# Optimization experiments

Hardware: AMD Instinct MI355X
Metric: run time of the kernel (lower is better)

Reference implementation:

```python
import jax, jax.numpy as jnp
import numpy as np

B, S, H, D = 4, 2048, 16, 64
E = H * D  # embedding_dim = 1024


def setup_inputs() -> dict:
    key = jax.random.key(0)
    ks = jax.random.split(key, 5)
    scale = 1.0 / np.sqrt(E)
    return {
        "x": jax.random.normal(ks[0], (B, S, E), dtype=jnp.float32),
        "wq": jax.random.normal(ks[1], (E, E), dtype=jnp.float32) * scale,
        "wk": jax.random.normal(ks[2], (E, E), dtype=jnp.float32) * scale,
        "wv": jax.random.normal(ks[3], (E, E), dtype=jnp.float32) * scale,
        "wo": jax.random.normal(ks[4], (E, E), dtype=jnp.float32) * scale,
    }


def reference(x, wq, wk, wv, wo):
    b, s, e = x.shape
    # nn.Linear: y = x @ W^T (no bias; use_bias=False)
    q = (x @ wq.T).reshape(b, s, H, D)
    k = (x @ wk.T).reshape(b, s, H, D)
    v = (x @ wv.T).reshape(b, s, H, D)
    # NOTE: original scales by sqrt(embedding_dim), not sqrt(head_dim)
    scores = jnp.einsum("bqhd,bkhd->bhqk", q, k) / jnp.sqrt(jnp.float32(e))
    causal = jnp.tril(jnp.ones((s, s), dtype=bool))  # mask[:s,:s]
    scores = jnp.where(causal, scores, -jnp.inf)
    attn = jax.nn.softmax(scores, axis=-1)
    out = jnp.einsum("bhql,blhd->bqhd", attn, v).reshape(b, s, e)
    return out @ wo.T
```

## Files before the change

### kernel.cpp

```cpp
#include <hip/hip_runtime.h>
#include <hip/hip_bf16.h>

#define E_DIM 1024
#define NHEAD 16
#define HDIM  64
#define BATCH 4
#define SEQ   2048
#define RQKV  (3 * E_DIM)

typedef __attribute__((ext_vector_type(8))) short bf16x8;
typedef __attribute__((ext_vector_type(4))) float f32x4;
typedef __attribute__((ext_vector_type(16))) float f32x16;

#define SCL2 0.04508422f

static __device__ __forceinline__ unsigned short bits_of(__hip_bfloat16 h) {
    return *reinterpret_cast<unsigned short*>(&h);
}

static __device__ __forceinline__ void gload_lds16(const void* g, void* l) {
    __builtin_amdgcn_global_load_lds(
        (__attribute__((address_space(1))) void*)g,
        (__attribute__((address_space(3))) void*)l, 16, 0, 0);
}

static __device__ __forceinline__ unsigned cvt_pk_bf16(float a, float b) {
    unsigned r;
    asm("v_cvt_pk_bf16_f32 %0, %1, %2" : "=v"(r) : "v"(a), "v"(b));
    return r;
}

static __device__ __forceinline__ float exp2_raw(float x) {
    float r;
    asm("v_exp_f32 %0, %1" : "=v"(r) : "v"(x));
    return r;
}

__global__ void cast_all_kernel(
    const float* __restrict__ x,  const float* __restrict__ wq,
    const float* __restrict__ wk, const float* __restrict__ wv,
    const float* __restrict__ wo,
    __hip_bfloat16* __restrict__ xb, __hip_bfloat16* __restrict__ wqkvb,
    __hip_bfloat16* __restrict__ wob) {
    const int NX4 = (BATCH * SEQ * E_DIM) / 4;
    const int NW4 = (E_DIM * E_DIM) / 4;
    int id = blockIdx.x * 256 + threadIdx.x;

    const float* in;
    __hip_bfloat16* out;
    float scl = 1.0f;
    if (id < NX4) {
        in = x; out = xb;
    } else {
        const int r = id - NX4;
        const int wsel = r >> 18;
        id = r & (NW4 - 1);
        switch (wsel) {
            case 0: in = wq; out = wqkvb;            scl = SCL2; break;
            case 1: in = wk; out = wqkvb + NW4 * 4;  break;
            case 2: in = wv; out = wqkvb + NW4 * 8;  break;
            default: in = wo; out = wob;             break;
        }
    }
    float4 v = reinterpret_cast<const float4*>(in)[id];
    ushort4 u;
    u.x = bits_of(__float2bfloat16(v.x * scl));
    u.y = bits_of(__float2bfloat16(v.y * scl));
    u.z = bits_of(__float2bfloat16(v.z * scl));
    u.w = bits_of(__float2bfloat16(v.w * scl));
    reinterpret_cast<ushort4*>(out)[id] = u;
}

template<int FN, int OUT_F32>
__global__ __launch_bounds__(512) void gemm_ph(
    const __hip_bfloat16* __restrict__ A,
    const __hip_bfloat16* __restrict__ Bw,
    void* __restrict__ Cv,
    int M, int N, int K) {
    constexpr int BN = FN * 64;
    __shared__ __align__(16) __hip_bfloat16 As[2][128 * 64];
    __shared__ __align__(16) __hip_bfloat16 Bs[2][BN * 64];

    const int nbx = gridDim.x;
    const int lin = blockIdx.y * nbx + blockIdx.x;
    const int cpx = (nbx * gridDim.y) >> 3;
    const int swz = (lin & 7) * cpx + (lin >> 3);
    const int mBase = (swz / nbx) * 128, nBase = (swz % nbx) * BN;

    const int t = threadIdx.x, lane = t & 63, w = t >> 6;
    const int wr = w >> 2, wc = w & 3;
    const int lr = lane & 15;
    const int lkb = (lane >> 4) * 16;

    f32x4 acc[4][FN];
#pragma unroll
    for (int i = 0; i < 4; ++i)
#pragma unroll
        for (int j = 0; j < FN; ++j) acc[i][j] = (f32x4){0.f, 0.f, 0.f, 0.f};

    const int NKT = K >> 6;

    auto STAGE = [&](int kt, int b) {
#pragma unroll
        for (int i = 0; i < 2; ++i) {
            const int q = i * 512 + t;
            const int r = q >> 3, cb = (q & 7) * 16;
            const char* src = (const char*)A +
                ((size_t)(mBase + r) * K + kt * 64) * 2 + (cb ^ ((r & 7) << 4));
            gload_lds16(src, (char*)&As[b][0] + q * 16);
        }
#pragma unroll
        for (int i = 0; i < FN; ++i) {
            const int q = i * 512 + t;
            const int r = q >> 3, cb = (q & 7) * 16;
            const char* src = (const char*)Bw +
                ((size_t)(nBase + r) * K + kt * 64) * 2 + (cb ^ ((r & 7) << 4));
            gload_lds16(src, (char*)&Bs[b][0] + q * 16);
        }
    };

    STAGE(0, 0);
    for (int kt = 0; kt < NKT; ++kt) {
        const int buf = kt & 1;
        asm volatile("s_waitcnt vmcnt(0)" ::: "memory");
        __builtin_amdgcn_s_barrier();
        __builtin_amdgcn_sched_barrier(0);

        bf16x8 bfr[FN][2];
#pragma unroll
        for (int fn = 0; fn < FN; ++fn)
#pragma unroll
            for (int ks = 0; ks < 2; ++ks) {
                const int R = wc * (FN * 16) + fn * 16 + lr;
                const int addr = R * 128 + ((ks * 64 + lkb) ^ ((R & 7) << 4));
                bfr[fn][ks] = *reinterpret_cast<const bf16x8*>(
                    (const char*)&Bs[buf][0] + addr);
            }
        {
            bf16x8 af[2][2];
#pragma unroll
            for (int f = 0; f < 2; ++f)
#pragma unroll
                for (int ks = 0; ks < 2; ++ks) {
                    const int R = wr * 64 + f * 16 + lr;
                    const int addr = R * 128 + ((ks * 64 + lkb) ^ ((R & 7) << 4));
                    af[f][ks] = *reinterpret_cast<const bf16x8*>(
                        (const char*)&As[buf][0] + addr);
                }
            if (kt + 1 < NKT) STAGE(kt + 1, buf ^ 1);
            __builtin_amdgcn_s_setprio(1);
#pragma unroll
            for (int f = 0; f < 2; ++f)
#pragma unroll
                for (int fn = 0; fn < FN; ++fn)
#pragma unroll
                    for (int ks = 0; ks < 2; ++ks)
                        acc[f][fn] = __builtin_amdgcn_mfma_f32_16x16x32_bf16(
                            af[f][ks], bfr[fn][ks], acc[f][fn], 0, 0, 0);
            __builtin_amdgcn_s_setprio(0);
        }
        {
            bf16x8 af[2][2];
#pragma unroll
            for (int f = 0; f < 2; ++f)
#pragma unroll
                for (int ks = 0; ks < 2; ++ks) {
                    const int R = wr * 64 + (f + 2) * 16 + lr;
                    const int addr = R * 128 + ((ks * 64 + lkb) ^ ((R & 7) << 4));
                    af[f][ks] = *reinterpret_cast<const bf16x8*>(
                        (const char*)&As[buf][0] + addr);
                }
            __builtin_amdgcn_s_setprio(1);
#pragma unroll
            for (int f = 0; f < 2; ++f)
#pragma unroll
                for (int fn = 0; fn < FN; ++fn)
#pragma unroll
                    for (int ks = 0; ks < 2; ++ks)
                        acc[f + 2][fn] = __builtin_amdgcn_mfma_f32_16x16x32_bf16(
                            af[f][ks], bfr[fn][ks], acc[f + 2][fn], 0, 0, 0);
            __builtin_amdgcn_s_setprio(0);
        }
    }

#pragma unroll
    for (int fm = 0; fm < 4; ++fm)
#pragma unroll
        for (int fn = 0; fn < FN; ++fn)
#pragma unroll
            for (int v = 0; v < 4; ++v) {
                const int row = mBase + wr * 64 + fm * 16 + (lane >> 4) * 4 + v;
                const int col = nBase + wc * (FN * 16) + fn * 16 + lr;
                if (OUT_F32)
                    ((float*)Cv)[(size_t)row * N + col] = acc[fm][fn][v];
                else
                    ((__hip_bfloat16*)Cv)[(size_t)row * N + col] =
                        __float2bfloat16(acc[fm][fn][v]);
            }
}

__global__ __launch_bounds__(256) void attn_kernel(
    const __hip_bfloat16* __restrict__ QKV,
    __hip_bfloat16* __restrict__ O) {
    __shared__ __align__(16) __hip_bfloat16 Kl[2][64][64];
    __shared__ __align__(16) __hip_bfloat16 Vt[2][64][64];

    const int t = threadIdx.x, w = t >> 6, lane = t & 63;
    const int lq = lane & 31, hi = lane >> 5;

    const int id = blockIdx.x;
    const int c = id & 7, k = id >> 3;
    const int bh = (k & 7) * 8 + c;
    const int qq = k >> 3;
    const int qb = (qq & 4) ? (qq < 8 ? qq + 4 : qq - 12) : 15 - qq;
    const int b = bh >> 4, h = bh & 15;

    const size_t rb = (size_t)b * SEQ;
    const __hip_bfloat16* Qg = QKV + rb * RQKV + h * HDIM;
    const __hip_bfloat16* Kg = QKV + rb * RQKV + E_DIM + h * HDIM;
    const __hip_bfloat16* Vg = QKV + rb * RQKV + 2 * E_DIM + h * HDIM;

    const int kst_row  = w * 16 + (lane >> 3);
    const int kst_slot = lane & 7;
    const int vkp = t & 31, vd0 = (t >> 5) * 8;

    const int qw0 = qb * 128 + w * 32;
    const int qg  = qw0 + lq;

    bf16x8 aq[4];
#pragma unroll
    for (int d0 = 0; d0 < 4; ++d0)
        aq[d0] = *reinterpret_cast<const bf16x8*>(
            Qg + (size_t)qg * RQKV + d0 * 16 + hi * 8);

    f32x16 oa[2];
#pragma unroll
    for (int m = 0; m < 2; ++m)
#pragma unroll
        for (int r = 0; r < 16; ++r) oa[m][r] = 0.f;
    float l_run = 0.f;

    const int NP = qb + 1;
    for (int pr = 0; pr < NP; ++pr) {
        const int k0a = pr * 128;
        __syncthreads();

#pragma unroll
        for (int half = 0; half < 2; ++half)
#pragma unroll
            for (int i = 0; i < 2; ++i) {
                const int r = kst_row + i * 8;
                const char* src =
                    (const char*)(Kg + (size_t)(k0a + half * 64 + r) * RQKV) +
                    ((kst_slot * 16) ^ ((r & 7) << 4));
                gload_lds16(src, &Kl[half][w * 16 + i * 8][0]);
            }
        {
            const __hip_bfloat16* vp0 =
                Vg + (size_t)(k0a + 2 * vkp) * RQKV + vd0;
            const __hip_bfloat16* vp1 = vp0 + (size_t)64 * RQKV;
            union { bf16x8 v; unsigned u[4]; } A0, B0, A1, B1;
            A0.v = *reinterpret_cast<const bf16x8*>(vp0);
            B0.v = *reinterpret_cast<const bf16x8*>(vp0 + RQKV);
            A1.v = *reinterpret_cast<const bf16x8*>(vp1);
            B1.v = *reinterpret_cast<const bf16x8*>(vp1 + RQKV);
            char* vt0 = reinterpret_cast<char*>(&Vt[0][0][0]);
            char* vt1 = reinterpret_cast<char*>(&Vt[1][0][0]);
#pragma unroll
            for (int jw = 0; jw < 4; ++jw) {
                const int da = vd0 + 2 * jw, db = da + 1;
                const int offa = da * 128 + ((vkp * 4) ^ ((da & 7) << 4));
                const int offb = db * 128 + ((vkp * 4) ^ ((db & 7) << 4));
                *reinterpret_cast<unsigned*>(vt0 + offa) =
                    __builtin_amdgcn_perm(B0.u[jw], A0.u[jw], 0x05040100u);
                *reinterpret_cast<unsigned*>(vt0 + offb) =
                    __builtin_amdgcn_perm(B0.u[jw], A0.u[jw], 0x07060302u);
                *reinterpret_cast<unsigned*>(vt1 + offa) =
                    __builtin_amdgcn_perm(B1.u[jw], A1.u[jw], 0x05040100u);
                *reinterpret_cast<unsigned*>(vt1 + offb) =
                    __builtin_amdgcn_perm(B1.u[jw], A1.u[jw], 0x07060302u);
            }
        }
        __syncthreads();

#pragma unroll
        for (int half = 0; half < 2; ++half) {
            const int k0 = k0a + half * 64;
            if (k0 > qw0 + 31) continue;

            f32x16 sc2[2];
            const char* klbase = (const char*)&Kl[half][0][0];
#pragma unroll
            for (int tt = 0; tt < 2; ++tt) {
#pragma unroll
                for (int r = 0; r < 16; ++r) sc2[tt][r] = 0.f;
                const int kr = tt * 32 + lq;
                const char* kbase = klbase + kr * 128;
                const int swz = (kr & 7) << 4;
#pragma unroll
                for (int d0 = 0; d0 < 4; ++d0) {
                    bf16x8 ak = *reinterpret_cast<const bf16x8*>(
                        kbase + ((d0 * 32 + hi * 16) ^ swz));
                    sc2[tt] = __builtin_amdgcn_mfma_f32_32x32x16_bf16(
                        ak, aq[d0], sc2[tt], 0, 0, 0);
                }
            }
            if (k0 + 63 > qw0) {
#pragma unroll
                for (int tt = 0; tt < 2; ++tt)
#pragma unroll
                    for (int r = 0; r < 16; ++r) {
                        const int kgl = k0 + tt * 32 +
                                        (r & 3) + 8 * (r >> 2) + 4 * hi;
                        if (kgl > qg) sc2[tt][r] = -1e30f;
                    }
            }
            float rsum = 0.f;
#pragma unroll
            for (int tt = 0; tt < 2; ++tt) {
                float s0 = 0.f, s1 = 0.f, s2 = 0.f, s3 = 0.f;
#pragma unroll
                for (int r = 0; r < 16; r += 4) {
                    float p0 = exp2_raw(sc2[tt][r]);
                    float p1 = exp2_raw(sc2[tt][r + 1]);
                    float p2 = exp2_raw(sc2[tt][r + 2]);
                    float p3 = exp2_raw(sc2[tt][r + 3]);
                    sc2[tt][r] = p0; sc2[tt][r + 1] = p1;
                    sc2[tt][r + 2] = p2; sc2[tt][r + 3] = p3;
                    s0 += p0; s1 += p1; s2 += p2; s3 += p3;
                }
                rsum += (s0 + s1) + (s2 + s3);
            }
            l_run += rsum;

            const char* vtbase = (const char*)&Vt[half][0][0];
#pragma unroll
            for (int tt = 0; tt < 2; ++tt)
#pragma unroll
                for (int sl = 0; sl < 2; ++sl) {
                    const int rbs = sl * 8;
                    const unsigned wA = cvt_pk_bf16(sc2[tt][rbs + 0], sc2[tt][rbs + 1]);
                    const unsigned wB = cvt_pk_bf16(sc2[tt][rbs + 2], sc2[tt][rbs + 3]);
                    const unsigned wC = cvt_pk_bf16(sc2[tt][rbs + 4], sc2[tt][rbs + 5]);
                    const unsigned wD = cvt_pk_bf16(sc2[tt][rbs + 6], sc2[tt][rbs + 7]);
                    const auto pA = __builtin_amdgcn_permlane32_swap(wA, wC, false, false);
                    const auto pB = __builtin_amdgcn_permlane32_swap(wB, wD, false, false);
                    union { unsigned u[4]; bf16x8 v; } pf;
                    pf.u[0] = pA[0]; pf.u[1] = pB[0];
                    pf.u[2] = pA[1]; pf.u[3] = pB[1];
                    const int ks = tt * 2 + sl;
#pragma unroll
                    for (int m = 0; m < 2; ++m) {
                        const int dr = m * 32 + lq;
                        bf16x8 av = *reinterpret_cast<const bf16x8*>(
                            vtbase + dr * 128 +
                            ((ks * 32 + hi * 16) ^ ((dr & 7) << 4)));
                        oa[m] = __builtin_amdgcn_mfma_f32_32x32x16_bf16(
                            av, pf.v, oa[m], 0, 0, 0);
                    }
                }
        }
    }

    l_run += __shfl_xor(l_run, 32);
    const float inv = 1.f / l_run;
    __hip_bfloat16* Orow = O + (rb + qg) * E_DIM + h * HDIM;
#pragma unroll
    for (int m = 0; m < 2; ++m)
#pragma unroll
        for (int q4 = 0; q4 < 4; ++q4) {
            ushort4 pk;
            pk.x = bits_of(__float2bfloat16(oa[m][q4 * 4 + 0] * inv));
            pk.y = bits_of(__float2bfloat16(oa[m][q4 * 4 + 1] * inv));
            pk.z = bits_of(__float2bfloat16(oa[m][q4 * 4 + 2] * inv));
            pk.w = bits_of(__float2bfloat16(oa[m][q4 * 4 + 3] * inv));
            *reinterpret_cast<ushort4*>(Orow + m * 32 + q4 * 8 + 4 * hi) = pk;
        }
}

extern "C" void kernel_launch(void* const* d_in, const int* in_sizes, int n_in,
                              void* d_out, int out_size, void* d_ws, size_t ws_size,
                              hipStream_t stream) {
    const float* x  = (const float*)d_in[0];
    const float* wq = (const float*)d_in[1];
    const float* wk = (const float*)d_in[2];
    const float* wv = (const float*)d_in[3];
    const float* wo = (const float*)d_in[4];

    const size_t SZ_X = (size_t)BATCH * SEQ * E_DIM;
    const size_t SZ_W = (size_t)E_DIM * E_DIM;

    char* p = (char*)d_ws;
    __hip_bfloat16* xb    = (__hip_bfloat16*)p; p += SZ_X * 2;
    __hip_bfloat16* wqkvb = (__hip_bfloat16*)p; p += 3 * SZ_W * 2;
    __hip_bfloat16* wob   = (__hip_bfloat16*)p; p += SZ_W * 2;
    __hip_bfloat16* QKVb  = (__hip_bfloat16*)p; p += SZ_X * 3 * 2;
    __hip_bfloat16* attb  = (__hip_bfloat16*)p; p += SZ_X * 2;

    cast_all_kernel<<<dim3(12288), 256, 0, stream>>>(
        x, wq, wk, wv, wo, xb, wqkvb, wob);

    const int M = BATCH * SEQ;
    gemm_ph<3, 0><<<dim3(RQKV / 192, M / 128), 512, 0, stream>>>(
        xb, wqkvb, QKVb, M, RQKV, E_DIM);

    attn_kernel<<<dim3(1024), 256, 0, stream>>>(QKVb, attb);

    gemm_ph<2, 1><<<dim3(E_DIM / 128, M / 128), 512, 0, stream>>>(
        attb, wob, d_out, M, E_DIM, E_DIM);
}
```

Before: 149.2 us.

## Shrink attention blocks to 64 queries with 2 waves and single K/V tile

Result: slower. 168.7 us (+13.1%).

```diff
diff --git a/kernel.cpp b/kernel.cpp
--- a/kernel.cpp
+++ b/kernel.cpp
@@ -199,20 +199,19 @@
             }
 }
 
-__global__ __launch_bounds__(256) void attn_kernel(
+__global__ __launch_bounds__(128) void attn_kernel(
     const __hip_bfloat16* __restrict__ QKV,
     __hip_bfloat16* __restrict__ O) {
-    __shared__ __align__(16) __hip_bfloat16 Kl[2][64][64];
-    __shared__ __align__(16) __hip_bfloat16 Vt[2][64][64];
+    __shared__ __align__(16) __hip_bfloat16 Kl[64][64];
+    __shared__ __align__(16) __hip_bfloat16 Vt[64][64];
 
     const int t = threadIdx.x, w = t >> 6, lane = t & 63;
     const int lq = lane & 31, hi = lane >> 5;
 
     const int id = blockIdx.x;
-    const int c = id & 7, k = id >> 3;
-    const int bh = (k & 7) * 8 + c;
-    const int qq = k >> 3;
-    const int qb = (qq & 4) ? (qq < 8 ? qq + 4 : qq - 12) : 15 - qq;
+    const int c = id & 7, j = id >> 3;
+    const int bh = (j & 7) * 8 + c;
+    const int qtile = j >> 3;
     const int b = bh >> 4, h = bh & 15;
 
     const size_t rb = (size_t)b * SEQ;
@@ -220,11 +219,10 @@
     const __hip_bfloat16* Kg = QKV + rb * RQKV + E_DIM + h * HDIM;
     const __hip_bfloat16* Vg = QKV + rb * RQKV + 2 * E_DIM + h * HDIM;
 
-    const int kst_row  = w * 16 + (lane >> 3);
-    const int kst_slot = lane & 7;
-    const int vkp = t & 31, vd0 = (t >> 5) * 8;
-
-    const int qw0 = qb * 128 + w * 32;
+    const int vkp = t & 31;
+    const int vdg = (t >> 5) * 16;
+
+    const int qw0 = qtile * 64 + w * 32;
     const int qg  = qw0 + lq;
 
     bf16x8 aq[4];
@@ -240,126 +238,110 @@
         for (int r = 0; r < 16; ++r) oa[m][r] = 0.f;
     float l_run = 0.f;
 
-    const int NP = qb + 1;
-    for (int pr = 0; pr < NP; ++pr) {
-        const int k0a = pr * 128;
+    const int NT = qtile + 1;
+    for (int kt = 0; kt < NT; ++kt) {
+        const int k0 = kt * 64;
         __syncthreads();
 
 #pragma unroll
-        for (int half = 0; half < 2; ++half)
-#pragma unroll
-            for (int i = 0; i < 2; ++i) {
-                const int r = kst_row + i * 8;
-                const char* src =
-                    (const char*)(Kg + (size_t)(k0a + half * 64 + r) * RQKV) +
-                    ((kst_slot * 16) ^ ((r & 7) << 4));
-                gload_lds16(src, &Kl[half][w * 16 + i * 8][0]);
-            }
+        for (int i = 0; i < 4; ++i) {
+            const int r = w * 32 + i * 8 + (lane >> 3);
+            const char* src = (const char*)(Kg + (size_t)(k0 + r) * RQKV) +
+                              (((lane & 7) * 16) ^ ((r & 7) << 4));
+            gload_lds16(src, &Kl[w * 32 + i * 8][0]);
+        }
         {
-            const __hip_bfloat16* vp0 =
-                Vg + (size_t)(k0a + 2 * vkp) * RQKV + vd0;
-            const __hip_bfloat16* vp1 = vp0 + (size_t)64 * RQKV;
-            union { bf16x8 v; unsigned u[4]; } A0, B0, A1, B1;
-            A0.v = *reinterpret_cast<const bf16x8*>(vp0);
-            B0.v = *reinterpret_cast<const bf16x8*>(vp0 + RQKV);
-            A1.v = *reinterpret_cast<const bf16x8*>(vp1);
-            B1.v = *reinterpret_cast<const bf16x8*>(vp1 + RQKV);
-            char* vt0 = reinterpret_cast<char*>(&Vt[0][0][0]);
-            char* vt1 = reinterpret_cast<char*>(&Vt[1][0][0]);
-#pragma unroll
-            for (int jw = 0; jw < 4; ++jw) {
-                const int da = vd0 + 2 * jw, db = da + 1;
-                const int offa = da * 128 + ((vkp * 4) ^ ((da & 7) << 4));
-                const int offb = db * 128 + ((vkp * 4) ^ ((db & 7) << 4));
-                *reinterpret_cast<unsigned*>(vt0 + offa) =
-                    __builtin_amdgcn_perm(B0.u[jw], A0.u[jw], 0x05040100u);
-                *reinterpret_cast<unsigned*>(vt0 + offb) =
-                    __builtin_amdgcn_perm(B0.u[jw], A0.u[jw], 0x07060302u);
-                *reinterpret_cast<unsigned*>(vt1 + offa) =
-                    __builtin_amdgcn_perm(B1.u[jw], A1.u[jw], 0x05040100u);
-                *reinterpret_cast<unsigned*>(vt1 + offb) =
-                    __builtin_amdgcn_perm(B1.u[jw], A1.u[jw], 0x07060302u);
+            const __hip_bfloat16* vp = Vg + (size_t)(k0 + 2 * vkp) * RQKV + vdg;
+            char* vt = reinterpret_cast<char*>(&Vt[0][0]);
+#pragma unroll
+            for (int o = 0; o < 2; ++o) {
+                union { bf16x8 v; unsigned u[4]; } Aa, Bb;
+                Aa.v = *reinterpret_cast<const bf16x8*>(vp + o * 8);
+                Bb.v = *reinterpret_cast<const bf16x8*>(vp + RQKV + o * 8);
+#pragma unroll
+                for (int jw = 0; jw < 4; ++jw) {
+                    const int da = vdg + o * 8 + 2 * jw, db = da + 1;
+                    *reinterpret_cast<unsigned*>(
+                        vt + da * 128 + ((vkp * 4) ^ ((da & 7) << 4))) =
+                        __builtin_amdgcn_perm(Bb.u[jw], Aa.u[jw], 0x05040100u);
+                    *reinterpret_cast<unsigned*>(
+                        vt + db * 128 + ((vkp * 4) ^ ((db & 7) << 4))) =
+                        __builtin_amdgcn_perm(Bb.u[jw], Aa.u[jw], 0x07060302u);
+                }
             }
         }
         __syncthreads();
 
-#pragma unroll
-        for (int half = 0; half < 2; ++half) {
-            const int k0 = k0a + half * 64;
-            if (k0 > qw0 + 31) continue;
-
-            f32x16 sc2[2];
-            const char* klbase = (const char*)&Kl[half][0][0];
-#pragma unroll
-            for (int tt = 0; tt < 2; ++tt) {
-#pragma unroll
-                for (int r = 0; r < 16; ++r) sc2[tt][r] = 0.f;
-                const int kr = tt * 32 + lq;
-                const char* kbase = klbase + kr * 128;
-                const int swz = (kr & 7) << 4;
-#pragma unroll
-                for (int d0 = 0; d0 < 4; ++d0) {
-                    bf16x8 ak = *reinterpret_cast<const bf16x8*>(
-                        kbase + ((d0 * 32 + hi * 16) ^ swz));
-                    sc2[tt] = __builtin_amdgcn_mfma_f32_32x32x16_bf16(
-                        ak, aq[d0], sc2[tt], 0, 0, 0);
-                }
-            }
-            if (k0 + 63 > qw0) {
-#pragma unroll
-                for (int tt = 0; tt < 2; ++tt)
-#pragma unroll
-                    for (int r = 0; r < 16; ++r) {
-                        const int kgl = k0 + tt * 32 +
-                                        (r & 3) + 8 * (r >> 2) + 4 * hi;
-                        if (kgl > qg) sc2[tt][r] = -1e30f;
-                    }
-            }
-            float rsum = 0.f;
-#pragma unroll
-            for (int tt = 0; tt < 2; ++tt) {
-                float s0 = 0.f, s1 = 0.f, s2 = 0.f, s3 = 0.f;
-#pragma unroll
-                for (int r = 0; r < 16; r += 4) {
-                    float p0 = exp2_raw(sc2[tt][r]);
-                    float p1 = exp2_raw(sc2[tt][r + 1]);
-                    float p2 = exp2_raw(sc2[tt][r + 2]);
-                    float p3 = exp2_raw(sc2[tt][r + 3]);
-                    sc2[tt][r] = p0; sc2[tt][r + 1] = p1;
-                    sc2[tt][r + 2] = p2; sc2[tt][r + 3] = p3;
-                    s0 += p0; s1 += p1; s2 += p2; s3 += p3;
-                }
-                rsum += (s0 + s1) + (s2 + s3);
-            }
-            l_run += rsum;
-
-            const char* vtbase = (const char*)&Vt[half][0][0];
+        f32x16 sc2[2];
+#pragma unroll
+        for (int tt = 0; tt < 2; ++tt) {
+#pragma unroll
+            for (int r = 0; r < 16; ++r) sc2[tt][r] = 0.f;
+            const int kr = tt * 32 + lq;
+            const char* kbase =
+                reinterpret_cast<const char*>(&Kl[0][0]) + kr * 128;
+            const int swz = (kr & 7) << 4;
+#pragma unroll
+            for (int d0 = 0; d0 < 4; ++d0) {
+                bf16x8 ak = *reinterpret_cast<const bf16x8*>(
+                    kbase + ((d0 * 32 + hi * 16) ^ swz));
+                sc2[tt] = __builtin_amdgcn_mfma_f32_32x32x16_bf16(
+                    ak, aq[d0], sc2[tt], 0, 0, 0);
+            }
+        }
+        if (k0 + 63 > qw0) {
 #pragma unroll
             for (int tt = 0; tt < 2; ++tt)
 #pragma unroll
-                for (int sl = 0; sl < 2; ++sl) {
-                    const int rbs = sl * 8;
-                    const unsigned wA = cvt_pk_bf16(sc2[tt][rbs + 0], sc2[tt][rbs + 1]);
-                    const unsigned wB = cvt_pk_bf16(sc2[tt][rbs + 2], sc2[tt][rbs + 3]);
-                    const unsigned wC = cvt_pk_bf16(sc2[tt][rbs + 4], sc2[tt][rbs + 5]);
-                    const unsigned wD = cvt_pk_bf16(sc2[tt][rbs + 6], sc2[tt][rbs + 7]);
-                    const auto pA = __builtin_amdgcn_permlane32_swap(wA, wC, false, false);
-                    const auto pB = __builtin_amdgcn_permlane32_swap(wB, wD, false, false);
-                    union { unsigned u[4]; bf16x8 v; } pf;
-                    pf.u[0] = pA[0]; pf.u[1] = pB[0];
-                    pf.u[2] = pA[1]; pf.u[3] = pB[1];
-                    const int ks = tt * 2 + sl;
-#pragma unroll
-                    for (int m = 0; m < 2; ++m) {
-                        const int dr = m * 32 + lq;
-                        bf16x8 av = *reinterpret_cast<const bf16x8*>(
-                            vtbase + dr * 128 +
-                            ((ks * 32 + hi * 16) ^ ((dr & 7) << 4)));
-                        oa[m] = __builtin_amdgcn_mfma_f32_32x32x16_bf16(
-                            av, pf.v, oa[m], 0, 0, 0);
-                    }
-                }
-        }
+                for (int r = 0; r < 16; ++r) {
+                    const int kgl = k0 + tt * 32 + (r & 3) + 8 * (r >> 2) + 4 * hi;
+                    if (kgl > qg) sc2[tt][r] = -1e30f;
+                }
+        }
+        float rsum = 0.f;
+#pragma unroll
+        for (int tt = 0; tt < 2; ++tt) {
+            float s0 = 0.f, s1 = 0.f, s2 = 0.f, s3 = 0.f;
+#pragma unroll
+            for (int r = 0; r < 16; r += 4) {
+                float p0 = exp2_raw(sc2[tt][r]);
+                float p1 = exp2_raw(sc2[tt][r + 1]);
+                float p2 = exp2_raw(sc2[tt][r + 2]);
+                float p3 = exp2_raw(sc2[tt][r + 3]);
+                sc2[tt][r] = p0; sc2[tt][r + 1] = p1;
+                sc2[tt][r + 2] = p2; sc2[tt][r + 3] = p3;
+                s0 += p0; s1 += p1; s2 += p2; s3 += p3;
+            }
+            rsum += (s0 + s1) + (s2 + s3);
+        }
+        l_run += rsum;
+
+        const char* vtbase = (const char*)&Vt[0][0];
+#pragma unroll
+        for (int tt = 0; tt < 2; ++tt)
+#pragma unroll
+            for (int sl = 0; sl < 2; ++sl) {
+                const int rbs = sl * 8;
+                const unsigned wA = cvt_pk_bf16(sc2[tt][rbs + 0], sc2[tt][rbs + 1]);
+                const unsigned wB = cvt_pk_bf16(sc2[tt][rbs + 2], sc2[tt][rbs + 3]);
+                const unsigned wC = cvt_pk_bf16(sc2[tt][rbs + 4], sc2[tt][rbs + 5]);
+                const unsigned wD = cvt_pk_bf16(sc2[tt][rbs + 6], sc2[tt][rbs + 7]);
+                const auto pA = __builtin_amdgcn_permlane32_swap(wA, wC, false, false);
+                const auto pB = __builtin_amdgcn_permlane32_swap(wB, wD, false, false);
+                union { unsigned u[4]; bf16x8 v; } pf;
+                pf.u[0] = pA[0]; pf.u[1] = pB[0];
+                pf.u[2] = pA[1]; pf.u[3] = pB[1];
+                const int ks = tt * 2 + sl;
+#pragma unroll
+                for (int m = 0; m < 2; ++m) {
+                    const int dr = m * 32 + lq;
+                    bf16x8 av = *reinterpret_cast<const bf16x8*>(
+                        vtbase + dr * 128 +
+                        ((ks * 32 + hi * 16) ^ ((dr & 7) << 4)));
+                    oa[m] = __builtin_amdgcn_mfma_f32_32x32x16_bf16(
+                        av, pf.v, oa[m], 0, 0, 0);
+                }
+            }
     }
 
     l_run += __shfl_xor(l_run, 32);
@@ -404,7 +386,7 @@
     gemm_ph<3, 0><<<dim3(RQKV / 192, M / 128), 512, 0, stream>>>(
         xb, wqkvb, QKVb, M, RQKV, E_DIM);
 
-    attn_kernel<<<dim3(1024), 256, 0, stream>>>(QKVb, attb);
+    attn_kernel<<<dim3(2048), 128, 0, stream>>>(QKVb, attb);
 
     gemm_ph<2, 1><<<dim3(E_DIM / 128, M / 128), 512, 0, stream>>>(
         attb, wob, d_out, M, E_DIM, E_DIM);
```
